# Optimization experiments

Hardware: AMD Instinct MI355X
Metric: run time of the kernel (lower is better)

## Reference

```python
import jax, jax.numpy as jnp
import numpy as np

MAX_ACF_LAG = 6
TOP_K_FFT = 3
CLIP_VALUE = 5.0
EPS = 1e-8


def setup_inputs() -> dict:
    key = jax.random.key(0)
    x = jax.random.normal(key, (128, 4096, 32), dtype=jnp.float32)
    return {"x": x}


def _per_var_features(x):
    # x: [B, T, V] -> [B, V, 10 + MAX_ACF_LAG]
    B, T, V = x.shape
    mean = jnp.mean(x, axis=1)                      # [B, V]
    xc = x - mean[:, None, :]                       # centered, [B, T, V]
    var = jnp.mean(xc * xc, axis=1)                 # [B, V]
    std = jnp.sqrt(var + EPS)
    z = xc / std[:, None, :]
    skew = jnp.mean(z ** 3, axis=1)
    kurt = jnp.mean(z ** 4, axis=1)
    mn = jnp.min(x, axis=1)
    mx = jnp.max(x, axis=1)
    # linear trend slope via least squares on t = 0..T-1
    t = jnp.arange(T, dtype=x.dtype)
    tc = t - jnp.mean(t)
    slope = jnp.einsum('btv,t->bv', xc, tc) / jnp.sum(tc * tc)
    # top-k FFT magnitudes (exclude DC), normalized by T
    mag = jnp.abs(jnp.fft.rfft(x, axis=1))[:, 1:, :] / T   # [B, F, V]
    topk, _ = jax.lax.top_k(jnp.transpose(mag, (0, 2, 1)), TOP_K_FFT)  # [B, V, k]
    # autocorrelation at lags 1..MAX_ACF_LAG
    denom = jnp.sum(xc * xc, axis=1) + EPS          # [B, V]
    acfs = [jnp.sum(xc[:, :-lag, :] * xc[:, lag:, :], axis=1) / denom
            for lag in range(1, MAX_ACF_LAG + 1)]
    acf = jnp.stack(acfs, axis=-1)                  # [B, V, L]
    base = jnp.stack([mean, std, skew, kurt, mn, mx, slope], axis=-1)  # [B, V, 7]
    return jnp.concatenate([base, topk, acf], axis=-1)  # [B, V, 16]


def reference(x):
    feats = _per_var_features(x)                    # [B, V, 16]
    f_mean = jnp.mean(feats, axis=1)                # [B, 16]
    f_std = jnp.std(feats, axis=1)                  # [B, 16]
    out = jnp.concatenate([f_mean, f_std], axis=-1) # [B, 32]
    return jnp.clip(out, -CLIP_VALUE, CLIP_VALUE)
```

## Files before the change

### kernel.cpp

```cpp
#include <hip/hip_runtime.h>
#include <math.h>

#define T_LEN 4096
#define M_LEN 2048
#define V_DIM 32
#define B_DIM 128
#define NTHREADS 512
#define NWAVES 8
#define NSERIES 4096
#define FS NSERIES

__device__ __forceinline__ int SW(int i) { return i ^ (((i >> 4) & 7) << 1); }

__device__ __forceinline__ int fpos(int k) {
    return ((k & 3) << 9) | (((k >> 2) & 3) << 7) | (((k >> 4) & 3) << 5)
         | (((k >> 6) & 3) << 3) | (((k >> 8) & 3) << 1) | ((k >> 10) & 1);
}

__device__ __forceinline__ void ins3(float& a0, float& a1, float& a2, float m) {
    if (m > a0) { a2 = a1; a1 = a0; a0 = m; }
    else if (m > a1) { a2 = a1; a1 = m; }
    else if (m > a2) { a2 = m; }
}

#define SCR_A_PART 0
#define SCR_A_FIN  48
#define SCR_B_PART 64
#define SCR_B_FIN  704
#define SCR_C_PART 724
#define SCR_SIZE   772

template <int ST>
__device__ __forceinline__ void fft_stage(float2* Z, int tid) {
    constexpr int lq = 9 - 2 * ST;
    constexpr int q  = 1 << lq;
    const float scale = -3.06796158e-3f * (float)(1 << (2 * ST));
    #pragma unroll
    for (int si = 0; si < 2; si++) {
        const int g = tid >> lq;
        const int j = tid & (q - 1);
        const int base = (si << 11) + (g << (lq + 2)) + j;
        const int p0 = SW(base), p1 = SW(base + q);
        const int p2i = SW(base + 2 * q), p3 = SW(base + 3 * q);
        float2 a = Z[p0], bb = Z[p1], c = Z[p2i], d = Z[p3];
        float t0r = a.x + c.x,  t0i = a.y + c.y;
        float t1r = a.x - c.x,  t1i = a.y - c.y;
        float t2r = bb.x + d.x, t2i = bb.y + d.y;
        float t3r = bb.x - d.x, t3i = bb.y - d.y;
        float sn, cs;
        __sincosf(scale * (float)j, &sn, &cs);
        float c2 = cs * cs - sn * sn, s2 = 2.f * cs * sn;
        float c3 = c2 * cs - s2 * sn, s3 = c2 * sn + s2 * cs;
        float y1r = t1r + t3i, y1i = t1i - t3r;
        float y2r = t0r - t2r, y2i = t0i - t2i;
        float y3r = t1r - t3i, y3i = t1i + t3r;
        Z[p0]  = make_float2(t0r + t2r, t0i + t2i);
        Z[p1]  = make_float2(y1r * cs - y1i * sn, y1r * sn + y1i * cs);
        Z[p2i] = make_float2(y2r * c2 - y2i * s2, y2r * s2 + y2i * c2);
        Z[p3]  = make_float2(y3r * c3 - y3i * s3, y3r * s3 + y3i * c3);
    }
}

__device__ __forceinline__ float2 rdpost(const float2* Z, int zb, int p) {
    int e = p & ~1;
    float4 v = *reinterpret_cast<const float4*>(&Z[zb + SW(e)]);
    return (p & 1) ? make_float2(v.x - v.z, v.y - v.w)
                   : make_float2(v.x + v.z, v.y + v.w);
}

__global__ __launch_bounds__(NTHREADS, 8)
void ts_feat_kernel(const float* __restrict__ x, float* __restrict__ feats) {
    __shared__ __align__(16) float data[2][T_LEN];
    __shared__ float scr[SCR_SIZE];
    float* const fd = &data[0][0];
    float2* const Z = reinterpret_cast<float2*>(fd);

    const int tid = threadIdx.x;
    const int bid  = blockIdx.x;
    const int xcd  = bid & 7;
    const int idx  = bid >> 3;
    const int b    = xcd + ((idx >> 4) << 3);
    const int pair = idx & 15;
    const int v0   = pair * 2;
    const int sid0 = b * V_DIM + v0;

    const float2* __restrict__ p2 =
        reinterpret_cast<const float2*>(x + (size_t)b * T_LEN * V_DIM + v0);

    float s0 = 0.f, s1 = 0.f;
    float mn0 = 3.4e38f, mn1 = 3.4e38f, mx0 = -3.4e38f, mx1 = -3.4e38f;
    const int comp = tid & 1;
    #pragma unroll
    for (int i = 0; i < 8; i++) {
        int t = tid + i * NTHREADS;
        float2 val = p2[(size_t)t * (V_DIM / 2)];
        int f = SW(t >> 1);
        fd[(f << 1) + comp] = val.x;
        fd[T_LEN + (f << 1) + comp] = val.y;
        s0 += val.x; s1 += val.y;
        mn0 = fminf(mn0, val.x); mn1 = fminf(mn1, val.y);
        mx0 = fmaxf(mx0, val.x); mx1 = fmaxf(mx1, val.y);
    }
    #pragma unroll
    for (int o = 32; o > 0; o >>= 1) {
        s0 += __shfl_down(s0, o); s1 += __shfl_down(s1, o);
        mn0 = fminf(mn0, __shfl_down(mn0, o)); mn1 = fminf(mn1, __shfl_down(mn1, o));
        mx0 = fmaxf(mx0, __shfl_down(mx0, o)); mx1 = fmaxf(mx1, __shfl_down(mx1, o));
    }
    const int lane = tid & 63, wv = tid >> 6;
    if (lane == 0) {
        float* p = &scr[SCR_A_PART + wv * 6];
        p[0] = s0; p[1] = s1; p[2] = mn0; p[3] = mn1; p[4] = mx0; p[5] = mx1;
    }
    __syncthreads();
    if (tid < 6) {
        float r = scr[SCR_A_PART + tid];
        #pragma unroll
        for (int w = 1; w < NWAVES; w++) {
            float v = scr[SCR_A_PART + w * 6 + tid];
            r = (tid < 2) ? (r + v) : ((tid < 4) ? fminf(r, v) : fmaxf(r, v));
        }
        scr[SCR_A_FIN + tid] = r;
    }
    __syncthreads();
    const float mean0 = scr[SCR_A_FIN + 0] * (1.f / T_LEN);
    const float mean1 = scr[SCR_A_FIN + 1] * (1.f / T_LEN);
    float fmn = 0.f, fmx = 0.f;
    if (tid < 2) { fmn = scr[SCR_A_FIN + 2 + tid]; fmx = scr[SCR_A_FIN + 4 + tid]; }

    #pragma unroll 1
    for (int si = 0; si < 2; si++) {
        const float m = si ? mean1 : mean0;
        const int fb = (si << 11) + (tid << 2);
        float4 q0 = *reinterpret_cast<const float4*>(&Z[SW(fb)]);
        float4 q1 = *reinterpret_cast<const float4*>(&Z[SW(fb + 2)]);
        float p1v = 0.f, p2v = 0.f, p3v = 0.f, p4v = 0.f, p5v = 0.f, p6v = 0.f;
        if (tid > 0) {
            float2 tv = Z[SW(fb - 3)];
            float4 tq = *reinterpret_cast<const float4*>(&Z[SW(fb - 2)]);
            p6v = tv.x - m; p5v = tv.y - m;
            p4v = tq.x - m; p3v = tq.y - m; p2v = tq.z - m; p1v = tq.w - m;
        }
        float acc[10];
        #pragma unroll
        for (int r = 0; r < 10; r++) acc[r] = 0.f;
        const float tf0 = (float)(tid * 8) - 2047.5f;
        float xs[8] = {q0.x, q0.y, q0.z, q0.w, q1.x, q1.y, q1.z, q1.w};
        #pragma unroll
        for (int u = 0; u < 8; u++) {
            float c = xs[u] - m;
            float c2v = c * c;
            acc[0] += c2v;
            acc[1] += c2v * c;
            acc[2] += c2v * c2v;
            acc[3] += c * (tf0 + (float)u);
            acc[4] += p1v * c; acc[5] += p2v * c; acc[6] += p3v * c;
            acc[7] += p4v * c; acc[8] += p5v * c; acc[9] += p6v * c;
            p6v = p5v; p5v = p4v; p4v = p3v; p3v = p2v; p2v = p1v; p1v = c;
        }
        #pragma unroll
        for (int r = 0; r < 10; r++) {
            acc[r] += __shfl_down(acc[r], 32);
            acc[r] += __shfl_down(acc[r], 16);
            acc[r] += __shfl_down(acc[r], 8);
            acc[r] += __shfl_down(acc[r], 4);
        }
        if (lane < 4) {
            #pragma unroll
            for (int r = 0; r < 10; r++)
                scr[SCR_B_PART + si * 320 + wv * 40 + lane * 10 + r] = acc[r];
        }
    }
    __syncthreads();

    if (tid < 10) {
        float s = 0.f;
        #pragma unroll
        for (int e = 0; e < 32; e++) s += scr[SCR_B_PART + e * 10 + tid];
        scr[SCR_B_FIN + tid] = s;
    } else if (tid >= 16 && tid < 26) {
        const int f = tid - 16;
        float s = 0.f;
        #pragma unroll
        for (int e = 0; e < 32; e++) s += scr[SCR_B_PART + 320 + e * 10 + f];
        scr[SCR_B_FIN + 10 + f] = s;
    }
    fft_stage<0>(Z, tid);
    __syncthreads();

    if (tid < 2) {
        const float* A = &scr[SCR_B_FIN + tid * 10];
        const float m = tid ? mean1 : mean0;
        float c2 = A[0], c3 = A[1], c4 = A[2], ct = A[3];
        float var = c2 * (1.f / T_LEN);
        float sd  = sqrtf(var + 1e-8f);
        float i3  = 1.f / (sd * sd * sd);
        float dn  = c2 + 1e-8f;
        float* fp = feats + (sid0 + tid);
        fp[0 * FS] = m; fp[1 * FS] = sd;
        fp[2 * FS] = c3 * (1.f / T_LEN) * i3;
        fp[3 * FS] = c4 * (1.f / T_LEN) * i3 / sd;
        fp[4 * FS] = fmn; fp[5 * FS] = fmx;
        fp[6 * FS] = ct / 5726622720.f;
        fp[10 * FS] = A[4] / dn; fp[11 * FS] = A[5] / dn; fp[12 * FS] = A[6] / dn;
        fp[13 * FS] = A[7] / dn; fp[14 * FS] = A[8] / dn; fp[15 * FS] = A[9] / dn;
    }
    fft_stage<1>(Z, tid);
    __syncthreads();
    fft_stage<2>(Z, tid);
    __syncthreads();
    fft_stage<3>(Z, tid);
    __syncthreads();
    fft_stage<4>(Z, tid);
    __syncthreads();

    const float inv_T = 1.f / (float)T_LEN;
    float a0 = -1.f, a1 = -1.f, a2 = -1.f;
    float b0 = -1.f, b1 = -1.f, b2 = -1.f;
    #pragma unroll
    for (int i = 0; i < 2; i++) {
        int k  = 1 + tid + (i << 9);
        int pa = fpos(k);
        int pb = fpos(M_LEN - k);
        const bool notself = (k != 1024);
        float ang = (float)k * (-3.14159265358979f / (float)M_LEN);
        float sn, cs; __sincosf(ang, &sn, &cs);
        {
            float2 Za = rdpost(Z, 0, pa), Zb = rdpost(Z, 0, pb);
            float Er = 0.5f * (Za.x + Zb.x), Ei = 0.5f * (Za.y - Zb.y);
            float Or = 0.5f * (Za.y + Zb.y), Oi = 0.5f * (Zb.x - Za.x);
            float u = cs * Or - sn * Oi, v = cs * Oi + sn * Or;
            float Xr = Er + u, Xi = Ei + v;
            ins3(a0, a1, a2, sqrtf(Xr * Xr + Xi * Xi));
            if (notself) {
                float Yr = Er - u, Yi = v - Ei;
                ins3(a0, a1, a2, sqrtf(Yr * Yr + Yi * Yi));
            }
        }
        {
            float2 Za = rdpost(Z, M_LEN, pa), Zb = rdpost(Z, M_LEN, pb);
            float Er = 0.5f * (Za.x + Zb.x), Ei = 0.5f * (Za.y - Zb.y);
            float Or = 0.5f * (Za.y + Zb.y), Oi = 0.5f * (Zb.x - Za.x);
            float u = cs * Or - sn * Oi, v = cs * Oi + sn * Or;
            float Xr = Er + u, Xi = Ei + v;
            ins3(b0, b1, b2, sqrtf(Xr * Xr + Xi * Xi));
            if (notself) {
                float Yr = Er - u, Yi = v - Ei;
                ins3(b0, b1, b2, sqrtf(Yr * Yr + Yi * Yi));
            }
        }
    }
    if (tid == 0) {
        float2 Z0 = rdpost(Z, 0, 0);
        ins3(a0, a1, a2, fabsf(Z0.x - Z0.y));
        float2 Z1 = rdpost(Z, M_LEN, 0);
        ins3(b0, b1, b2, fabsf(Z1.x - Z1.y));
    }
    #pragma unroll
    for (int o = 32; o > 0; o >>= 1) {
        float u0 = __shfl_down(a0, o), u1 = __shfl_down(a1, o), u2 = __shfl_down(a2, o);
        ins3(a0, a1, a2, u0); ins3(a0, a1, a2, u1); ins3(a0, a1, a2, u2);
        float w0 = __shfl_down(b0, o), w1 = __shfl_down(b1, o), w2 = __shfl_down(b2, o);
        ins3(b0, b1, b2, w0); ins3(b0, b1, b2, w1); ins3(b0, b1, b2, w2);
    }
    if (lane == 0) {
        float* p = &scr[SCR_C_PART + wv * 6];
        p[0] = a0; p[1] = a1; p[2] = a2; p[3] = b0; p[4] = b1; p[5] = b2;
    }
    __syncthreads();
    if (tid < 2) {
        const int off = SCR_C_PART + tid * 3;
        float t0 = scr[off], t1 = scr[off + 1], t2 = scr[off + 2];
        #pragma unroll
        for (int w = 1; w < NWAVES; w++) {
            ins3(t0, t1, t2, scr[off + w * 6]);
            ins3(t0, t1, t2, scr[off + w * 6 + 1]);
            ins3(t0, t1, t2, scr[off + w * 6 + 2]);
        }
        float* fp = feats + (sid0 + tid);
        fp[7 * FS] = t0 * inv_T; fp[8 * FS] = t1 * inv_T; fp[9 * FS] = t2 * inv_T;
    }
}

__global__ __launch_bounds__(256)
void ts_reduce_kernel(const float* __restrict__ feats, float* __restrict__ out) {
    const int tid = threadIdx.x;
    const int lane = tid & 63;
    const int wid = blockIdx.x * 4 + (tid >> 6);
    const int pairidx = wid * 2 + (lane >> 5);
    const int b = pairidx >> 4, f = pairidx & 15;
    const int v = lane & 31;
    float val = feats[f * FS + b * V_DIM + v];
    float s = val;
    #pragma unroll
    for (int o = 16; o > 0; o >>= 1) s += __shfl_xor(s, o);
    float m = s * (1.f / V_DIM);
    float d = val - m;
    float q = d * d;
    #pragma unroll
    for (int o = 16; o > 0; o >>= 1) q += __shfl_xor(q, o);
    float sd = sqrtf(q * (1.f / V_DIM));
    if (v == 0) {
        out[b * 32 + f]      = fminf(fmaxf(m,  -5.f), 5.f);
        out[b * 32 + 16 + f] = fminf(fmaxf(sd, -5.f), 5.f);
    }
}

extern "C" void kernel_launch(void* const* d_in, const int* in_sizes, int n_in,
                              void* d_out, int out_size, void* d_ws, size_t ws_size,
                              hipStream_t stream) {
    const float* x = (const float*)d_in[0];
    float* out = (float*)d_out;
    float* feats = (float*)d_ws;

    hipLaunchKernelGGL(ts_feat_kernel, dim3(B_DIM * V_DIM / 2), dim3(NTHREADS), 0, stream,
                       x, feats);
    hipLaunchKernelGGL(ts_reduce_kernel, dim3(256), dim3(256), 0, stream,
                       feats, out);
}
```

Measured before the change: 146.7 us.

## Process one series per 256-thread block instead of two per 512-thread block

Each block now handles a single variable's time series with 256 threads, holding 16 contiguous samples per thread in registers. The x loads go from paired float2 to scalar strided loads, and the register copy is reused directly for the statistics pass without rereading shared memory. The FFT stages and post-processing loops are remapped so each thread covers two butterflies or four bins of a single series. This halves shared memory per block and doubles the grid size. The cost is narrower 4-byte global loads with a stride of 32 floats, which may lower coalescing efficiency.

```diff
diff --git a/kernel.cpp b/kernel.cpp
--- a/kernel.cpp
+++ b/kernel.cpp
@@ -5,8 +5,8 @@
 #define M_LEN 2048
 #define V_DIM 32
 #define B_DIM 128
-#define NTHREADS 512
-#define NWAVES 8
+#define NTHREADS 256
+#define NWAVES 4
 #define NSERIES 4096
 #define FS NSERIES
 
@@ -24,11 +24,11 @@
 }
 
 #define SCR_A_PART 0
-#define SCR_A_FIN  48
-#define SCR_B_PART 64
-#define SCR_B_FIN  704
-#define SCR_C_PART 724
-#define SCR_SIZE   772
+#define SCR_A_FIN  12
+#define SCR_B_PART 16
+#define SCR_B_FIN  176
+#define SCR_C_PART 186
+#define SCR_SIZE   200
 
 template <int ST>
 __device__ __forceinline__ void fft_stage(float2* Z, int tid) {
@@ -36,10 +36,15 @@
     constexpr int q  = 1 << lq;
     const float scale = -3.06796158e-3f * (float)(1 << (2 * ST));
     #pragma unroll
-    for (int si = 0; si < 2; si++) {
-        const int g = tid >> lq;
-        const int j = tid & (q - 1);
-        const int base = (si << 11) + (g << (lq + 2)) + j;
+    for (int i = 0; i < 2; i++) {
+        const int w = tid + (i << 8);
+        const int g = w >> lq;
+        const int j = w & (q - 1);
+        float sn, cs;
+        __sincosf(scale * (float)j, &sn, &cs);
+        const float c2 = cs * cs - sn * sn, s2 = 2.f * cs * sn;
+        const float c3 = c2 * cs - s2 * sn, s3 = c2 * sn + s2 * cs;
+        const int base = (g << (lq + 2)) + j;
         const int p0 = SW(base), p1 = SW(base + q);
         const int p2i = SW(base + 2 * q), p3 = SW(base + 3 * q);
         float2 a = Z[p0], bb = Z[p1], c = Z[p2i], d = Z[p3];
@@ -47,10 +52,6 @@
         float t1r = a.x - c.x,  t1i = a.y - c.y;
         float t2r = bb.x + d.x, t2i = bb.y + d.y;
         float t3r = bb.x - d.x, t3i = bb.y - d.y;
-        float sn, cs;
-        __sincosf(scale * (float)j, &sn, &cs);
-        float c2 = cs * cs - sn * sn, s2 = 2.f * cs * sn;
-        float c3 = c2 * cs - s2 * sn, s3 = c2 * sn + s2 * cs;
         float y1r = t1r + t3i, y1i = t1i - t3r;
         float y2r = t0r - t2r, y2i = t0i - t2i;
         float y3r = t1r - t3i, y3i = t1i + t3r;
@@ -61,146 +62,129 @@
     }
 }
 
-__device__ __forceinline__ float2 rdpost(const float2* Z, int zb, int p) {
+__device__ __forceinline__ float2 rdpost(const float2* Z, int p) {
     int e = p & ~1;
-    float4 v = *reinterpret_cast<const float4*>(&Z[zb + SW(e)]);
+    float4 v = *reinterpret_cast<const float4*>(&Z[SW(e)]);
     return (p & 1) ? make_float2(v.x - v.z, v.y - v.w)
                    : make_float2(v.x + v.z, v.y + v.w);
 }
 
 __global__ __launch_bounds__(NTHREADS, 8)
 void ts_feat_kernel(const float* __restrict__ x, float* __restrict__ feats) {
-    __shared__ __align__(16) float data[2][T_LEN];
+    __shared__ __align__(16) float data[T_LEN];
     __shared__ float scr[SCR_SIZE];
-    float* const fd = &data[0][0];
-    float2* const Z = reinterpret_cast<float2*>(fd);
+    float2* const Z = reinterpret_cast<float2*>(&data[0]);
 
     const int tid = threadIdx.x;
-    const int bid  = blockIdx.x;
-    const int xcd  = bid & 7;
-    const int idx  = bid >> 3;
-    const int b    = xcd + ((idx >> 4) << 3);
-    const int pair = idx & 15;
-    const int v0   = pair * 2;
-    const int sid0 = b * V_DIM + v0;
-
-    const float2* __restrict__ p2 =
-        reinterpret_cast<const float2*>(x + (size_t)b * T_LEN * V_DIM + v0);
-
-    float s0 = 0.f, s1 = 0.f;
-    float mn0 = 3.4e38f, mn1 = 3.4e38f, mx0 = -3.4e38f, mx1 = -3.4e38f;
-    const int comp = tid & 1;
-    #pragma unroll
-    for (int i = 0; i < 8; i++) {
-        int t = tid + i * NTHREADS;
-        float2 val = p2[(size_t)t * (V_DIM / 2)];
-        int f = SW(t >> 1);
-        fd[(f << 1) + comp] = val.x;
-        fd[T_LEN + (f << 1) + comp] = val.y;
-        s0 += val.x; s1 += val.y;
-        mn0 = fminf(mn0, val.x); mn1 = fminf(mn1, val.y);
-        mx0 = fmaxf(mx0, val.x); mx1 = fmaxf(mx1, val.y);
+    const int bid = blockIdx.x;
+    const int xcd = bid & 7;
+    const int idx = bid >> 3;
+    const int b   = xcd + ((idx >> 5) << 3);
+    const int v   = idx & 31;
+    const int sid = b * V_DIM + v;
+
+    const float* __restrict__ px = x + (size_t)b * T_LEN * V_DIM + v;
+
+    float xr[16];
+    #pragma unroll
+    for (int u = 0; u < 16; u++) {
+        xr[u] = px[(size_t)(16 * tid + u) * V_DIM];
+    }
+    float s = 0.f, mn = 3.4e38f, mx = -3.4e38f;
+    #pragma unroll
+    for (int u = 0; u < 16; u++) {
+        s += xr[u]; mn = fminf(mn, xr[u]); mx = fmaxf(mx, xr[u]);
+    }
+    const int fb2 = tid * 8;
+    #pragma unroll
+    for (int u4 = 0; u4 < 4; u4++) {
+        float4 q = make_float4(xr[4 * u4], xr[4 * u4 + 1], xr[4 * u4 + 2], xr[4 * u4 + 3]);
+        *reinterpret_cast<float4*>(&Z[SW(fb2 + 2 * u4)]) = q;
     }
     #pragma unroll
     for (int o = 32; o > 0; o >>= 1) {
-        s0 += __shfl_down(s0, o); s1 += __shfl_down(s1, o);
-        mn0 = fminf(mn0, __shfl_down(mn0, o)); mn1 = fminf(mn1, __shfl_down(mn1, o));
-        mx0 = fmaxf(mx0, __shfl_down(mx0, o)); mx1 = fmaxf(mx1, __shfl_down(mx1, o));
+        s += __shfl_down(s, o);
+        mn = fminf(mn, __shfl_down(mn, o));
+        mx = fmaxf(mx, __shfl_down(mx, o));
     }
     const int lane = tid & 63, wv = tid >> 6;
     if (lane == 0) {
-        float* p = &scr[SCR_A_PART + wv * 6];
-        p[0] = s0; p[1] = s1; p[2] = mn0; p[3] = mn1; p[4] = mx0; p[5] = mx1;
-    }
-    __syncthreads();
-    if (tid < 6) {
+        scr[SCR_A_PART + wv * 3 + 0] = s;
+        scr[SCR_A_PART + wv * 3 + 1] = mn;
+        scr[SCR_A_PART + wv * 3 + 2] = mx;
+    }
+    __syncthreads();
+    if (tid < 3) {
         float r = scr[SCR_A_PART + tid];
         #pragma unroll
         for (int w = 1; w < NWAVES; w++) {
-            float v = scr[SCR_A_PART + w * 6 + tid];
-            r = (tid < 2) ? (r + v) : ((tid < 4) ? fminf(r, v) : fmaxf(r, v));
+            float vv = scr[SCR_A_PART + w * 3 + tid];
+            r = (tid == 0) ? (r + vv) : ((tid == 1) ? fminf(r, vv) : fmaxf(r, vv));
         }
         scr[SCR_A_FIN + tid] = r;
     }
     __syncthreads();
-    const float mean0 = scr[SCR_A_FIN + 0] * (1.f / T_LEN);
-    const float mean1 = scr[SCR_A_FIN + 1] * (1.f / T_LEN);
-    float fmn = 0.f, fmx = 0.f;
-    if (tid < 2) { fmn = scr[SCR_A_FIN + 2 + tid]; fmx = scr[SCR_A_FIN + 4 + tid]; }
-
-    #pragma unroll 1
-    for (int si = 0; si < 2; si++) {
-        const float m = si ? mean1 : mean0;
-        const int fb = (si << 11) + (tid << 2);
-        float4 q0 = *reinterpret_cast<const float4*>(&Z[SW(fb)]);
-        float4 q1 = *reinterpret_cast<const float4*>(&Z[SW(fb + 2)]);
+    const float m = scr[SCR_A_FIN + 0] * (1.f / T_LEN);
+
+    {
+        float q2 = 0.f, q3 = 0.f, q4 = 0.f, qt = 0.f;
+        float l1 = 0.f, l2 = 0.f, l3 = 0.f, l4 = 0.f, l5 = 0.f, l6 = 0.f;
         float p1v = 0.f, p2v = 0.f, p3v = 0.f, p4v = 0.f, p5v = 0.f, p6v = 0.f;
         if (tid > 0) {
-            float2 tv = Z[SW(fb - 3)];
-            float4 tq = *reinterpret_cast<const float4*>(&Z[SW(fb - 2)]);
+            float2 tv = Z[SW(fb2 - 3)];
+            float4 tq = *reinterpret_cast<const float4*>(&Z[SW(fb2 - 2)]);
             p6v = tv.x - m; p5v = tv.y - m;
             p4v = tq.x - m; p3v = tq.y - m; p2v = tq.z - m; p1v = tq.w - m;
         }
-        float acc[10];
-        #pragma unroll
-        for (int r = 0; r < 10; r++) acc[r] = 0.f;
-        const float tf0 = (float)(tid * 8) - 2047.5f;
-        float xs[8] = {q0.x, q0.y, q0.z, q0.w, q1.x, q1.y, q1.z, q1.w};
-        #pragma unroll
-        for (int u = 0; u < 8; u++) {
-            float c = xs[u] - m;
-            float c2v = c * c;
-            acc[0] += c2v;
-            acc[1] += c2v * c;
-            acc[2] += c2v * c2v;
-            acc[3] += c * (tf0 + (float)u);
-            acc[4] += p1v * c; acc[5] += p2v * c; acc[6] += p3v * c;
-            acc[7] += p4v * c; acc[8] += p5v * c; acc[9] += p6v * c;
+        const float tf0 = (float)(tid * 16) - 2047.5f;
+        #pragma unroll
+        for (int u = 0; u < 16; u++) {
+            float c = xr[u] - m;
+            float cc = c * c;
+            q2 += cc; q3 += cc * c; q4 += cc * cc;
+            qt += c * (tf0 + (float)u);
+            l1 += p1v * c; l2 += p2v * c; l3 += p3v * c;
+            l4 += p4v * c; l5 += p5v * c; l6 += p6v * c;
             p6v = p5v; p5v = p4v; p4v = p3v; p3v = p2v; p2v = p1v; p1v = c;
         }
         #pragma unroll
-        for (int r = 0; r < 10; r++) {
-            acc[r] += __shfl_down(acc[r], 32);
-            acc[r] += __shfl_down(acc[r], 16);
-            acc[r] += __shfl_down(acc[r], 8);
-            acc[r] += __shfl_down(acc[r], 4);
+        for (int o = 32; o >= 4; o >>= 1) {
+            q2 += __shfl_down(q2, o); q3 += __shfl_down(q3, o);
+            q4 += __shfl_down(q4, o); qt += __shfl_down(qt, o);
+            l1 += __shfl_down(l1, o); l2 += __shfl_down(l2, o);
+            l3 += __shfl_down(l3, o); l4 += __shfl_down(l4, o);
+            l5 += __shfl_down(l5, o); l6 += __shfl_down(l6, o);
         }
         if (lane < 4) {
-            #pragma unroll
-            for (int r = 0; r < 10; r++)
-                scr[SCR_B_PART + si * 320 + wv * 40 + lane * 10 + r] = acc[r];
+            float* part = &scr[SCR_B_PART + wv * 40 + lane * 10];
+            part[0] = q2; part[1] = q3; part[2] = q4; part[3] = qt;
+            part[4] = l1; part[5] = l2; part[6] = l3;
+            part[7] = l4; part[8] = l5; part[9] = l6;
         }
     }
     __syncthreads();
 
     if (tid < 10) {
-        float s = 0.f;
-        #pragma unroll
-        for (int e = 0; e < 32; e++) s += scr[SCR_B_PART + e * 10 + tid];
-        scr[SCR_B_FIN + tid] = s;
-    } else if (tid >= 16 && tid < 26) {
-        const int f = tid - 16;
-        float s = 0.f;
-        #pragma unroll
-        for (int e = 0; e < 32; e++) s += scr[SCR_B_PART + 320 + e * 10 + f];
-        scr[SCR_B_FIN + 10 + f] = s;
+        float acc = 0.f;
+        #pragma unroll
+        for (int e = 0; e < 16; e++) acc += scr[SCR_B_PART + e * 10 + tid];
+        scr[SCR_B_FIN + tid] = acc;
     }
     fft_stage<0>(Z, tid);
     __syncthreads();
 
-    if (tid < 2) {
-        const float* A = &scr[SCR_B_FIN + tid * 10];
-        const float m = tid ? mean1 : mean0;
+    if (tid == 0) {
+        const float* A = &scr[SCR_B_FIN];
         float c2 = A[0], c3 = A[1], c4 = A[2], ct = A[3];
         float var = c2 * (1.f / T_LEN);
         float sd  = sqrtf(var + 1e-8f);
         float i3  = 1.f / (sd * sd * sd);
         float dn  = c2 + 1e-8f;
-        float* fp = feats + (sid0 + tid);
+        float* fp = feats + sid;
         fp[0 * FS] = m; fp[1 * FS] = sd;
         fp[2 * FS] = c3 * (1.f / T_LEN) * i3;
         fp[3 * FS] = c4 * (1.f / T_LEN) * i3 / sd;
-        fp[4 * FS] = fmn; fp[5 * FS] = fmx;
+        fp[4 * FS] = scr[SCR_A_FIN + 1]; fp[5 * FS] = scr[SCR_A_FIN + 2];
         fp[6 * FS] = ct / 5726622720.f;
         fp[10 * FS] = A[4] / dn; fp[11 * FS] = A[5] / dn; fp[12 * FS] = A[6] / dn;
         fp[13 * FS] = A[7] / dn; fp[14 * FS] = A[8] / dn; fp[15 * FS] = A[9] / dn;
@@ -216,68 +200,48 @@
 
     const float inv_T = 1.f / (float)T_LEN;
     float a0 = -1.f, a1 = -1.f, a2 = -1.f;
-    float b0 = -1.f, b1 = -1.f, b2 = -1.f;
-    #pragma unroll
-    for (int i = 0; i < 2; i++) {
-        int k  = 1 + tid + (i << 9);
+    #pragma unroll
+    for (int i = 0; i < 4; i++) {
+        int k  = 1 + tid + (i << 8);
         int pa = fpos(k);
         int pb = fpos(M_LEN - k);
-        const bool notself = (k != 1024);
         float ang = (float)k * (-3.14159265358979f / (float)M_LEN);
         float sn, cs; __sincosf(ang, &sn, &cs);
-        {
-            float2 Za = rdpost(Z, 0, pa), Zb = rdpost(Z, 0, pb);
-            float Er = 0.5f * (Za.x + Zb.x), Ei = 0.5f * (Za.y - Zb.y);
-            float Or = 0.5f * (Za.y + Zb.y), Oi = 0.5f * (Zb.x - Za.x);
-            float u = cs * Or - sn * Oi, v = cs * Oi + sn * Or;
-            float Xr = Er + u, Xi = Ei + v;
-            ins3(a0, a1, a2, sqrtf(Xr * Xr + Xi * Xi));
-            if (notself) {
-                float Yr = Er - u, Yi = v - Ei;
-                ins3(a0, a1, a2, sqrtf(Yr * Yr + Yi * Yi));
-            }
-        }
-        {
-            float2 Za = rdpost(Z, M_LEN, pa), Zb = rdpost(Z, M_LEN, pb);
-            float Er = 0.5f * (Za.x + Zb.x), Ei = 0.5f * (Za.y - Zb.y);
-            float Or = 0.5f * (Za.y + Zb.y), Oi = 0.5f * (Zb.x - Za.x);
-            float u = cs * Or - sn * Oi, v = cs * Oi + sn * Or;
-            float Xr = Er + u, Xi = Ei + v;
-            ins3(b0, b1, b2, sqrtf(Xr * Xr + Xi * Xi));
-            if (notself) {
-                float Yr = Er - u, Yi = v - Ei;
-                ins3(b0, b1, b2, sqrtf(Yr * Yr + Yi * Yi));
-            }
+        float2 Za = rdpost(Z, pa), Zb = rdpost(Z, pb);
+        float Er = 0.5f * (Za.x + Zb.x), Ei = 0.5f * (Za.y - Zb.y);
+        float Or = 0.5f * (Za.y + Zb.y), Oi = 0.5f * (Zb.x - Za.x);
+        float u = cs * Or - sn * Oi, vv = cs * Oi + sn * Or;
+        float Xr = Er + u, Xi = Ei + vv;
+        ins3(a0, a1, a2, sqrtf(Xr * Xr + Xi * Xi));
+        if (k != 1024) {
+            float Yr = Er - u, Yi = vv - Ei;
+            ins3(a0, a1, a2, sqrtf(Yr * Yr + Yi * Yi));
         }
     }
     if (tid == 0) {
-        float2 Z0 = rdpost(Z, 0, 0);
+        float2 Z0 = rdpost(Z, 0);
         ins3(a0, a1, a2, fabsf(Z0.x - Z0.y));
-        float2 Z1 = rdpost(Z, M_LEN, 0);
-        ins3(b0, b1, b2, fabsf(Z1.x - Z1.y));
     }
     #pragma unroll
     for (int o = 32; o > 0; o >>= 1) {
         float u0 = __shfl_down(a0, o), u1 = __shfl_down(a1, o), u2 = __shfl_down(a2, o);
         ins3(a0, a1, a2, u0); ins3(a0, a1, a2, u1); ins3(a0, a1, a2, u2);
-        float w0 = __shfl_down(b0, o), w1 = __shfl_down(b1, o), w2 = __shfl_down(b2, o);
-        ins3(b0, b1, b2, w0); ins3(b0, b1, b2, w1); ins3(b0, b1, b2, w2);
     }
     if (lane == 0) {
-        float* p = &scr[SCR_C_PART + wv * 6];
-        p[0] = a0; p[1] = a1; p[2] = a2; p[3] = b0; p[4] = b1; p[5] = b2;
-    }
-    __syncthreads();
-    if (tid < 2) {
-        const int off = SCR_C_PART + tid * 3;
-        float t0 = scr[off], t1 = scr[off + 1], t2 = scr[off + 2];
+        scr[SCR_C_PART + wv * 3 + 0] = a0;
+        scr[SCR_C_PART + wv * 3 + 1] = a1;
+        scr[SCR_C_PART + wv * 3 + 2] = a2;
+    }
+    __syncthreads();
+    if (tid == 0) {
+        float t0 = scr[SCR_C_PART], t1 = scr[SCR_C_PART + 1], t2 = scr[SCR_C_PART + 2];
         #pragma unroll
         for (int w = 1; w < NWAVES; w++) {
-            ins3(t0, t1, t2, scr[off + w * 6]);
-            ins3(t0, t1, t2, scr[off + w * 6 + 1]);
-            ins3(t0, t1, t2, scr[off + w * 6 + 2]);
-        }
-        float* fp = feats + (sid0 + tid);
+            ins3(t0, t1, t2, scr[SCR_C_PART + w * 3 + 0]);
+            ins3(t0, t1, t2, scr[SCR_C_PART + w * 3 + 1]);
+            ins3(t0, t1, t2, scr[SCR_C_PART + w * 3 + 2]);
+        }
+        float* fp = feats + sid;
         fp[7 * FS] = t0 * inv_T; fp[8 * FS] = t1 * inv_T; fp[9 * FS] = t2 * inv_T;
     }
 }
@@ -313,7 +277,7 @@
     float* out = (float*)d_out;
     float* feats = (float*)d_ws;
 
-    hipLaunchKernelGGL(ts_feat_kernel, dim3(B_DIM * V_DIM / 2), dim3(NTHREADS), 0, stream,
+    hipLaunchKernelGGL(ts_feat_kernel, dim3(NSERIES), dim3(NTHREADS), 0, stream,
                        x, feats);
     hipLaunchKernelGGL(ts_reduce_kernel, dim3(256), dim3(256), 0, stream,
                        feats, out);
```

After: 125.3 us. -14.6%, faster.
